# Kernel optimization log

Measured on AMD Instinct MI355X. Metric: run time of the kernel, lower is better.

## Reference

```python
import jax, jax.numpy as jnp
import numpy as np

N = 50000      # nodes
E = 400000     # edges (before self loops)
IN = 128       # in_channels
H = 4          # num_heads (layers 1-2)
C = 32         # hidden_dim per head
HID = H * C    # 128 total hidden
CLS = 40       # num_classes (out_heads = 1)
EPS = 1e-5     # BatchNorm eps
SLOPE = 0.2    # LeakyReLU negative slope (PyG GATConv default)


def setup_inputs() -> dict:
    key = jax.random.key(0)
    ks = jax.random.split(key, 24)
    rn = lambda k, shp, s: jax.random.normal(k, shp, jnp.float32) * s
    x = jax.random.normal(ks[0], (N, IN), jnp.float32)
    src = jax.random.randint(ks[1], (E,), 0, N)
    dst = jax.random.randint(ks[2], (E,), 0, N)
    src = jnp.where(src == dst, (src + 1) % N, src)  # no pre-existing self loops
    edge_index = jnp.stack([src, dst]).astype(jnp.int32)
    inp = dict(x=x, edge_index=edge_index)
    # conv1: in IN -> H heads x C
    inp['W1'] = rn(ks[3], (IN, H * C), 1.0 / np.sqrt(IN))
    inp['as1'] = rn(ks[4], (H, C), 0.1)
    inp['ad1'] = rn(ks[5], (H, C), 0.1)
    inp['b1'] = rn(ks[6], (H * C,), 0.02)
    # conv2: HID -> H x C
    inp['W2'] = rn(ks[7], (HID, H * C), 1.0 / np.sqrt(HID))
    inp['as2'] = rn(ks[8], (H, C), 0.1)
    inp['ad2'] = rn(ks[9], (H, C), 0.1)
    inp['b2'] = rn(ks[10], (H * C,), 0.02)
    # conv3: HID -> 1 head x CLS, concat=False
    inp['W3'] = rn(ks[11], (HID, CLS), 1.0 / np.sqrt(HID))
    inp['as3'] = rn(ks[12], (1, CLS), 0.1)
    inp['ad3'] = rn(ks[13], (1, CLS), 0.1)
    inp['b3'] = rn(ks[14], (CLS,), 0.02)
    # residual projection
    inp['Wres'] = rn(ks[15], (IN, HID), 1.0 / np.sqrt(IN))
    # BatchNorm (eval mode: running stats)
    inp['g1'] = 1.0 + rn(ks[16], (HID,), 0.1)
    inp['be1'] = rn(ks[17], (HID,), 0.1)
    inp['m1'] = rn(ks[18], (HID,), 0.1)
    inp['v1'] = 1.0 + jax.random.uniform(ks[19], (HID,), jnp.float32) * 0.5
    inp['g2'] = 1.0 + rn(ks[20], (HID,), 0.1)
    inp['be2'] = rn(ks[21], (HID,), 0.1)
    inp['m2'] = rn(ks[22], (HID,), 0.1)
    inp['v2'] = 1.0 + jax.random.uniform(ks[23], (HID,), jnp.float32) * 0.5
    return inp


def _gat_conv(h, src, dst, W, a_src, a_dst, bias, heads, out_ch, concat):
    """PyG-style GATConv (eval: attention dropout off), self loops already in src/dst."""
    n = h.shape[0]
    xw = (h @ W).reshape(n, heads, out_ch)                    # [N,H,C]
    e_src = jnp.sum(xw * a_src, axis=-1)                      # [N,H]
    e_dst = jnp.sum(xw * a_dst, axis=-1)                      # [N,H]
    e = jax.nn.leaky_relu(e_src[src] + e_dst[dst], SLOPE)     # [E',H]
    # segment softmax over incoming edges of each dst node
    mseg = jax.ops.segment_max(e, dst, num_segments=n)        # [N,H]
    ex = jnp.exp(e - mseg[dst])
    den = jax.ops.segment_sum(ex, dst, num_segments=n)
    alpha = ex / den[dst]                                     # [E',H]
    out = jax.ops.segment_sum(alpha[:, :, None] * xw[src], dst, num_segments=n)  # [N,H,C]
    out = out.reshape(n, heads * out_ch) if concat else out.mean(axis=1)
    return out + bias


def _bn(h, g, b, m, v):
    return (h - m) * jax.lax.rsqrt(v + EPS) * g + b


def reference(x, edge_index, W1, as1, ad1, b1, W2, as2, ad2, b2,
              W3, as3, ad3, b3, Wres, g1, be1, m1, v1, g2, be2, m2, v2):
    n = x.shape[0]
    loop = jnp.arange(n, dtype=edge_index.dtype)
    src = jnp.concatenate([edge_index[0], loop])  # add self loops (PyG default)
    dst = jnp.concatenate([edge_index[1], loop])
    x0 = x
    h = _gat_conv(x0, src, dst, W1, as1, ad1, b1, H, C, True)
    h = jax.nn.elu(_bn(h, g1, be1, m1, v1) + x0 @ Wres)
    h_res = h
    h = _gat_conv(h, src, dst, W2, as2, ad2, b2, H, C, True)
    h = jax.nn.elu(_bn(h, g2, be2, m2, v2) + h_res)
    logits = _gat_conv(h, src, dst, W3, as3, ad3, b3, 1, CLS, False)
    return logits
```

## Files before the change

### kernel.cpp

```cpp
#include <hip/hip_runtime.h>
#include <hip/hip_bf16.h>

#define THREADS 256

typedef __attribute__((ext_vector_type(8))) short bfrag;
typedef __attribute__((ext_vector_type(4))) float f32x4;

__device__ inline unsigned short f2b(float v) {
    __hip_bfloat16 b = __float2bfloat16(v);
    return *reinterpret_cast<unsigned short*>(&b);
}
__device__ inline float b2f(unsigned short u) {
    return __uint_as_float(((unsigned)u) << 16);
}
__device__ inline float rdv(const void* p, int off, bool isbf) {
    return isbf ? b2f(((const unsigned short*)p)[off]) : ((const float*)p)[off];
}

__global__ void detect_kernel(const unsigned short* __restrict__ x, int n, int* flag) {
    __shared__ int cnt;
    if (threadIdx.x == 0) cnt = 0;
    __syncthreads();
    int local = 0;
    for (int i = threadIdx.x; i < n; i += THREADS) {
        unsigned ex = (x[i] >> 7) & 0xFF;
        if (ex == 0xFF || ex >= 134 || (ex > 0 && ex <= 100)) local++;
    }
    atomicAdd(&cnt, local);
    __syncthreads();
    if (threadIdx.x == 0) *flag = (cnt * 8 > n) ? 0 : 1;
}

struct InPtrs { const void* p[23]; };

__global__ void prep_kernel(InPtrs in, const int* __restrict__ flag,
                            unsigned short* __restrict__ Wl1, unsigned short* __restrict__ Wl2,
                            unsigned short* __restrict__ WlR, unsigned short* __restrict__ Wl3,
                            float* __restrict__ bnsc1, float* __restrict__ bnsh1,
                            float* __restrict__ bnsc2, float* __restrict__ bnsh2,
                            float* __restrict__ AS1f, float* __restrict__ AD1f,
                            float* __restrict__ AS2f, float* __restrict__ AD2f,
                            float* __restrict__ AS3f, float* __restrict__ AD3f,
                            float* __restrict__ B3f, unsigned short* __restrict__ xb,
                            int N, const int* __restrict__ ei, int* __restrict__ deg,
                            int E, int CB) {
    bool isbf = (*flag != 0);
    int b = blockIdx.x;
    if (b < 27) {
        const void* Wv; unsigned short* o; int cols, tt;
        if (b < 8)       { Wv = in.p[2];  o = Wl1; cols = 128; tt = b; }
        else if (b < 16) { Wv = in.p[6];  o = Wl2; cols = 128; tt = b - 8; }
        else if (b < 24) { Wv = in.p[14]; o = WlR; cols = 128; tt = b - 16; }
        else             { Wv = in.p[10]; o = Wl3; cols = 40;  tt = b - 24; }
        int id = tt * 256 + threadIdx.x;
        int t = id >> 8, ks = (id >> 6) & 3, l = id & 63;
        int q = l >> 4, n = l & 15;
        int c = t * 16 + n;
#pragma unroll
        for (int j = 0; j < 8; ++j) {
            int k = ks * 32 + q * 8 + j;
            float v = (c < cols) ? rdv(Wv, k * cols + c, isbf) : 0.f;
            o[id * 8 + j] = f2b(v);
        }
    } else if (b == 27) {
        int c = threadIdx.x;
        if (c < 128) {
            float s = rdv(in.p[15], c, isbf) * rsqrtf(rdv(in.p[18], c, isbf) + 1e-5f);
            bnsc1[c] = s;
            bnsh1[c] = rdv(in.p[16], c, isbf) - rdv(in.p[17], c, isbf) * s +
                       rdv(in.p[5], c, isbf) * s;
            AS1f[c] = rdv(in.p[3], c, isbf);
            AD1f[c] = rdv(in.p[4], c, isbf);
            AS2f[c] = rdv(in.p[7], c, isbf);
            AD2f[c] = rdv(in.p[8], c, isbf);
        } else {
            int d = c - 128;
            float s = rdv(in.p[19], d, isbf) * rsqrtf(rdv(in.p[22], d, isbf) + 1e-5f);
            bnsc2[d] = s;
            bnsh2[d] = rdv(in.p[20], d, isbf) - rdv(in.p[21], d, isbf) * s +
                       rdv(in.p[9], d, isbf) * s;
            if (d < 40) {
                AS3f[d] = rdv(in.p[11], d, isbf);
                AD3f[d] = rdv(in.p[12], d, isbf);
                B3f[d] = rdv(in.p[13], d, isbf);
            }
        }
    } else if (b < 28 + CB) {
        int i = (b - 28) * 256 + threadIdx.x;
        if (i < E + N) {
            int d = (i < E) ? ei[E + i] : (i - E);
            atomicAdd(&deg[d], 1);
        }
    } else {
        if (isbf) return;
        const float* xf = (const float*)in.p[0];
        int total = N * 128;
        int stride = (gridDim.x - 28 - CB) * 256;
        for (int i = (b - 28 - CB) * 256 + threadIdx.x; i < total; i += stride)
            xb[i] = f2b(xf[i]);
    }
}

__global__ void bsum_kernel(const int* __restrict__ deg, int* __restrict__ bsum, int N) {
    int idx = blockIdx.x * 256 + threadIdx.x;
    int lane = threadIdx.x & 63, wv = threadIdx.x >> 6;
    int v = (idx < N) ? deg[idx] : 0;
#pragma unroll
    for (int o = 1; o < 64; o <<= 1) v += __shfl_xor(v, o, 64);
    __shared__ int ws[4];
    if (lane == 0) ws[wv] = v;
    __syncthreads();
    if (threadIdx.x == 0) bsum[blockIdx.x] = ws[0] + ws[1] + ws[2] + ws[3];
}

__global__ __launch_bounds__(1024) void bscan_kernel(const int* __restrict__ bsum,
                                                     int* __restrict__ boff, int nb) {
    __shared__ int ws[16];
    int tid = threadIdx.x, lane = tid & 63, wv = tid >> 6;
    int v = (tid < nb) ? bsum[tid] : 0;
    int sc = v;
#pragma unroll
    for (int o = 1; o < 64; o <<= 1) {
        int t = __shfl_up(sc, o, 64);
        if (lane >= o) sc += t;
    }
    if (lane == 63) ws[wv] = sc;
    __syncthreads();
    int add = 0;
#pragma unroll
    for (int k = 0; k < 16; ++k) add += (k < wv) ? ws[k] : 0;
    if (tid < nb) boff[tid] = add + sc - v;
}

__global__ void scanw_kernel(const int* __restrict__ deg, const int* __restrict__ boff,
                             int* __restrict__ row_ptr, int* __restrict__ pos, int N) {
    int idx = blockIdx.x * 256 + threadIdx.x;
    int lane = threadIdx.x & 63, wv = threadIdx.x >> 6;
    int v = (idx < N) ? deg[idx] : 0;
    int sc = v;
#pragma unroll
    for (int o = 1; o < 64; o <<= 1) {
        int t = __shfl_up(sc, o, 64);
        if (lane >= o) sc += t;
    }
    __shared__ int ws[4];
    if (lane == 63) ws[wv] = sc;
    __syncthreads();
    int add = boff[blockIdx.x];
#pragma unroll
    for (int k = 0; k < 4; ++k) add += (k < wv) ? ws[k] : 0;
    int excl = add + sc - v;
    if (idx < N) {
        pos[idx] = excl;
        row_ptr[idx + 1] = excl + v;
    }
    if (idx == 0) row_ptr[0] = 0;
}

__global__ void scatter_kernel(const int* __restrict__ ei, int* __restrict__ pos,
                               int* __restrict__ csr, int E, int N) {
    int e = blockIdx.x * THREADS + threadIdx.x;
    if (e >= E + N) return;
    int s, d;
    if (e < E) { s = ei[e]; d = ei[E + e]; }
    else { s = e - E; d = s; }
    int p = atomicAdd(&pos[d], 1);
    csr[p] = s;
}

template <int COLT, int HEADS, bool ES>
__global__ __launch_bounds__(256) void gemm_mfma(
    const unsigned short* __restrict__ A, const unsigned short* __restrict__ Wg,
    const float* __restrict__ as_f, const float* __restrict__ ad_f,
    unsigned short* __restrict__ out, int ldc, int cols,
    float* __restrict__ es, float* __restrict__ ed, int N) {
    __shared__ __align__(16) unsigned short Wls[COLT * 2048];
    int tid = threadIdx.x;
    {
        const float4* src = (const float4*)Wg;
        float4* dst = (float4*)Wls;
#pragma unroll
        for (int i = 0; i < COLT; ++i) dst[tid + i * 256] = src[tid + i * 256];
    }
    __syncthreads();
    int w = tid >> 6, lane = tid & 63;
    int n = lane & 15, q = lane >> 4;
    int row0 = blockIdx.x * 64 + w * 16;
    int ar = row0 + n; ar = ar < N ? ar : N - 1;
    f32x4 acc[COLT];
#pragma unroll
    for (int t = 0; t < COLT; ++t) acc[t] = (f32x4){0.f, 0.f, 0.f, 0.f};
    const unsigned short* arow = A + (size_t)ar * 128;
#pragma unroll
    for (int ks = 0; ks < 4; ++ks) {
        bfrag a = *reinterpret_cast<const bfrag*>(arow + ks * 32 + q * 8);
#pragma unroll
        for (int t = 0; t < COLT; ++t) {
            bfrag b = *reinterpret_cast<const bfrag*>(&Wls[((t * 4 + ks) * 64 + lane) * 8]);
            acc[t] = __builtin_amdgcn_mfma_f32_16x16x32_bf16(a, b, acc[t], 0, 0, 0);
        }
    }
    if (ES) {
        float asv[COLT], adv[COLT];
#pragma unroll
        for (int t = 0; t < COLT; ++t) {
            int c = t * 16 + n;
            asv[t] = (c < cols) ? as_f[c] : 0.f;
            adv[t] = (c < cols) ? ad_f[c] : 0.f;
        }
#pragma unroll
        for (int r = 0; r < 4; ++r) {
            float pe[HEADS], pd[HEADS];
#pragma unroll
            for (int h = 0; h < HEADS; ++h) { pe[h] = 0.f; pd[h] = 0.f; }
#pragma unroll
            for (int t = 0; t < COLT; ++t) {
                int h = (HEADS == 4) ? (t >> 1) : 0;
                pe[h] = fmaf(acc[t][r], asv[t], pe[h]);
                pd[h] = fmaf(acc[t][r], adv[t], pd[h]);
            }
#pragma unroll
            for (int h = 0; h < HEADS; ++h) {
#pragma unroll
                for (int o = 1; o < 16; o <<= 1) {
                    pe[h] += __shfl_xor(pe[h], o, 64);
                    pd[h] += __shfl_xor(pd[h], o, 64);
                }
            }
            int row = row0 + q * 4 + r;
            if (n == 0 && row < N) {
#pragma unroll
                for (int h = 0; h < HEADS; ++h) {
                    es[(size_t)row * HEADS + h] = pe[h];
                    ed[(size_t)row * HEADS + h] = pd[h];
                }
            }
        }
    }
#pragma unroll
    for (int t = 0; t < COLT; ++t) {
        int col = t * 16 + n;
        if (col < cols) {
#pragma unroll
            for (int r = 0; r < 4; ++r) {
                int row = row0 + q * 4 + r;
                if (row < N) out[(size_t)row * ldc + col] = f2b(acc[t][r]);
            }
        }
    }
}

__global__ __launch_bounds__(256) void gemm_dual(
    const unsigned short* __restrict__ Araw, const unsigned short* __restrict__ Acvt,
    const int* __restrict__ flag,
    const unsigned short* __restrict__ Wg1, const unsigned short* __restrict__ WgR,
    const float* __restrict__ as_f, const float* __restrict__ ad_f,
    unsigned short* __restrict__ xwb, unsigned short* __restrict__ resb,
    float* __restrict__ es, float* __restrict__ ed, int N) {
    __shared__ __align__(16) unsigned short Wls[16 * 2048];
    int tid = threadIdx.x;
    {
        const float4* s1 = (const float4*)Wg1;
        const float4* s2 = (const float4*)WgR;
        float4* dst = (float4*)Wls;
#pragma unroll
        for (int i = 0; i < 8; ++i) dst[tid + i * 256] = s1[tid + i * 256];
#pragma unroll
        for (int i = 0; i < 8; ++i) dst[2048 + tid + i * 256] = s2[tid + i * 256];
    }
    const unsigned short* A = (*flag) ? Araw : Acvt;
    __syncthreads();
    int w = tid >> 6, lane = tid & 63;
    int n = lane & 15, q = lane >> 4;
    int row0 = blockIdx.x * 64 + w * 16;
    int ar = row0 + n; ar = ar < N ? ar : N - 1;
    f32x4 acc[16];
#pragma unroll
    for (int t = 0; t < 16; ++t) acc[t] = (f32x4){0.f, 0.f, 0.f, 0.f};
    const unsigned short* arow = A + (size_t)ar * 128;
#pragma unroll
    for (int ks = 0; ks < 4; ++ks) {
        bfrag a = *reinterpret_cast<const bfrag*>(arow + ks * 32 + q * 8);
#pragma unroll
        for (int t = 0; t < 8; ++t) {
            bfrag b = *reinterpret_cast<const bfrag*>(&Wls[((t * 4 + ks) * 64 + lane) * 8]);
            acc[t] = __builtin_amdgcn_mfma_f32_16x16x32_bf16(a, b, acc[t], 0, 0, 0);
        }
#pragma unroll
        for (int t = 0; t < 8; ++t) {
            bfrag b = *reinterpret_cast<const bfrag*>(&Wls[16384 + ((t * 4 + ks) * 64 + lane) * 8]);
            acc[8 + t] = __builtin_amdgcn_mfma_f32_16x16x32_bf16(a, b, acc[8 + t], 0, 0, 0);
        }
    }
    float asv[8], adv[8];
#pragma unroll
    for (int t = 0; t < 8; ++t) {
        int c = t * 16 + n;
        asv[t] = as_f[c];
        adv[t] = ad_f[c];
    }
#pragma unroll
    for (int r = 0; r < 4; ++r) {
        float pe[4] = {0.f, 0.f, 0.f, 0.f}, pd[4] = {0.f, 0.f, 0.f, 0.f};
#pragma unroll
        for (int t = 0; t < 8; ++t) {
            int h = t >> 1;
            pe[h] = fmaf(acc[t][r], asv[t], pe[h]);
            pd[h] = fmaf(acc[t][r], adv[t], pd[h]);
        }
#pragma unroll
        for (int h = 0; h < 4; ++h) {
#pragma unroll
            for (int o = 1; o < 16; o <<= 1) {
                pe[h] += __shfl_xor(pe[h], o, 64);
                pd[h] += __shfl_xor(pd[h], o, 64);
            }
        }
        int row = row0 + q * 4 + r;
        if (n == 0 && row < N) {
#pragma unroll
            for (int h = 0; h < 4; ++h) {
                es[(size_t)row * 4 + h] = pe[h];
                ed[(size_t)row * 4 + h] = pd[h];
            }
        }
    }
#pragma unroll
    for (int t = 0; t < 8; ++t) {
        int col = t * 16 + n;
#pragma unroll
        for (int r = 0; r < 4; ++r) {
            int row = row0 + q * 4 + r;
            if (row < N) {
                xwb[(size_t)row * 128 + col] = f2b(acc[t][r]);
                resb[(size_t)row * 128 + col] = f2b(acc[8 + t][r]);
            }
        }
    }
}

__global__ __launch_bounds__(256) void agg128_fused(
    const unsigned short* __restrict__ xwb, const float* __restrict__ es,
    const float* __restrict__ ed, const int* __restrict__ row_ptr,
    const int* __restrict__ csr, const float* __restrict__ bnsc,
    const float* __restrict__ bnsh, const unsigned short* __restrict__ resb,
    unsigned short* __restrict__ outb, int N) {
    int w = threadIdx.x >> 6, lane = threadIdx.x & 63;
    int node = blockIdx.x * 4 + w;
    if (node >= N) return;
    int h = lane >> 4;
    int i16 = lane & 15;
    int base = lane & 48;
    int c0 = lane * 2;
    float edl = ed[node * 4 + h];
    int start = __builtin_amdgcn_readfirstlane(row_ptr[node]);
    int end = __builtin_amdgcn_readfirstlane(row_ptr[node + 1]);
    float den = 0.f, a0 = 0.f, a1 = 0.f;
    for (int jb = start; jb < end; jb += 16) {
        int cnt = end - jb; cnt = cnt < 16 ? cnt : 16;
        cnt = __builtin_amdgcn_readfirstlane(cnt);
        int idx = jb + i16;
        int sv = csr[idx < end ? idx : end - 1];
        unsigned uu[16];
#pragma unroll
        for (int u = 0; u < 16; ++u) {
            if (u < cnt) {
                int s = __shfl(sv, u, 64);
                uu[u] = *(const unsigned*)(xwb + (size_t)s * 128 + c0);
            }
        }
        float wgl = 0.f;
        if (i16 < cnt) {
            float e = es[sv * 4 + h] + edl;
            e = e > 0.f ? e : 0.2f * e;
            wgl = __expf(e);
        }
        float d = wgl;
        d += __shfl_xor(d, 1, 64);
        d += __shfl_xor(d, 2, 64);
        d += __shfl_xor(d, 4, 64);
        d += __shfl_xor(d, 8, 64);
        den += d;
#pragma unroll
        for (int u = 0; u < 16; ++u) {
            if (u < cnt) {
                float wg = __shfl(wgl, base + u, 64);
                a0 = fmaf(wg, __uint_as_float(uu[u] << 16), a0);
                a1 = fmaf(wg, __uint_as_float(uu[u] & 0xffff0000u), a1);
            }
        }
    }
    float inv = 1.f / den;
    float2 sc = *(const float2*)(bnsc + c0);
    float2 sh = *(const float2*)(bnsh + c0);
    unsigned ur = *(const unsigned*)(resb + (size_t)node * 128 + c0);
    float v0 = fmaf(a0 * inv, sc.x, sh.x) + __uint_as_float(ur << 16);
    float v1 = fmaf(a1 * inv, sc.y, sh.y) + __uint_as_float(ur & 0xffff0000u);
    v0 = v0 > 0.f ? v0 : expm1f(v0);
    v1 = v1 > 0.f ? v1 : expm1f(v1);
    unsigned pk = (unsigned)f2b(v0) | ((unsigned)f2b(v1) << 16);
    *(unsigned*)(outb + (size_t)node * 128 + c0) = pk;
}

__global__ __launch_bounds__(256) void agg40_kernel(
    const unsigned short* __restrict__ xw3b, const float* __restrict__ es3,
    const float* __restrict__ ed3, const int* __restrict__ row_ptr,
    const int* __restrict__ csr, const float* __restrict__ b3,
    void* __restrict__ out, const int* __restrict__ flag, int N) {
    int w = threadIdx.x >> 6, lane = threadIdx.x & 63;
    int node = blockIdx.x * 4 + w;
    if (node >= N) return;
    int i16 = lane & 15;
    int g = lane >= 40 ? 2 : (lane >= 20 ? 1 : 0);
    int cp = lane - g * 20;
    int c0 = cp * 2; c0 = c0 > 38 ? 38 : c0;
    float edl = ed3[node];
    int start = __builtin_amdgcn_readfirstlane(row_ptr[node]);
    int end = __builtin_amdgcn_readfirstlane(row_ptr[node + 1]);
    float den = 0.f, a0 = 0.f, a1 = 0.f;
    for (int jb = start; jb < end; jb += 16) {
        int cnt = end - jb; cnt = cnt < 16 ? cnt : 16;
        cnt = __builtin_amdgcn_readfirstlane(cnt);
        int idx = jb + i16;
        int sv = csr[idx < end ? idx : end - 1];
        unsigned uu[6];
#pragma unroll
        for (int t = 0; t < 6; ++t) {
            int slot = 3 * t + g;
            if (slot < cnt) {
                int s = __shfl(sv, slot, 64);
                uu[t] = *(const unsigned*)(xw3b + (size_t)s * 40 + c0);
            }
        }
        float wgl = 0.f;
        if (i16 < cnt) {
            float e = es3[sv] + edl;
            e = e > 0.f ? e : 0.2f * e;
            wgl = __expf(e);
        }
        float d = wgl;
        d += __shfl_xor(d, 1, 64);
        d += __shfl_xor(d, 2, 64);
        d += __shfl_xor(d, 4, 64);
        d += __shfl_xor(d, 8, 64);
        den += d;
#pragma unroll
        for (int t = 0; t < 6; ++t) {
            int slot = 3 * t + g;
            if (slot < cnt) {
                float wg = __shfl(wgl, slot, 64);
                a0 = fmaf(wg, __uint_as_float(uu[t] << 16), a0);
                a1 = fmaf(wg, __uint_as_float(uu[t] & 0xffff0000u), a1);
            }
        }
    }
    float t0 = __shfl(a0, (lane + 20) & 63, 64);
    float t1 = __shfl(a0, (lane + 40) & 63, 64);
    float u0 = __shfl(a1, (lane + 20) & 63, 64);
    float u1 = __shfl(a1, (lane + 40) & 63, 64);
    a0 += t0 + t1;
    a1 += u0 + u1;
    if (lane < 20) {
        float inv = 1.f / den;
        float v0 = a0 * inv + b3[c0];
        float v1 = a1 * inv + b3[c0 + 1];
        size_t eoff = (size_t)node * 40 + c0;
        if (*flag) {
            unsigned pk = (unsigned)f2b(v0) | ((unsigned)f2b(v1) << 16);
            *(unsigned*)((unsigned short*)out + eoff) = pk;
        } else {
            *(float2*)((float*)out + eoff) = make_float2(v0, v1);
        }
    }
}

extern "C" void kernel_launch(void* const* d_in, const int* in_sizes, int n_in,
                              void* d_out, int out_size, void* d_ws, size_t ws_size,
                              hipStream_t stream) {
    (void)n_in; (void)out_size; (void)ws_size;
    const int N = in_sizes[0] / 128;
    const int E = in_sizes[1] / 2;
    const int EPN = E + N;
    const int NB = (N + 255) / 256;
    const int CB = (EPN + 255) / 256;
    char* base = (char*)d_ws;
    size_t off = 0;
    auto alloc = [&](size_t bytes) -> char* {
        char* p = base + off;
        off = (off + bytes + 255) & ~(size_t)255;
        return p;
    };
    int* flag = (int*)alloc(4);
    int* deg = (int*)alloc((size_t)N * 4);
    int* row_ptr = (int*)alloc((size_t)(N + 1) * 4);
    int* pos = (int*)alloc((size_t)N * 4);
    int* bsum = (int*)alloc((size_t)NB * 4);
    int* boff = (int*)alloc((size_t)NB * 4);
    int* csr = (int*)alloc((size_t)EPN * 4);
    float* bnsc1 = (float*)alloc(512); float* bnsh1 = (float*)alloc(512);
    float* bnsc2 = (float*)alloc(512); float* bnsh2 = (float*)alloc(512);
    float* AS1f = (float*)alloc(512); float* AD1f = (float*)alloc(512);
    float* AS2f = (float*)alloc(512); float* AD2f = (float*)alloc(512);
    float* AS3f = (float*)alloc(256); float* AD3f = (float*)alloc(256);
    float* B3f = (float*)alloc(256);
    unsigned short* Wl1 = (unsigned short*)alloc(32768);
    unsigned short* Wl2 = (unsigned short*)alloc(32768);
    unsigned short* WlR = (unsigned short*)alloc(32768);
    unsigned short* Wl3 = (unsigned short*)alloc(12288);
    unsigned short* xb = (unsigned short*)alloc((size_t)N * 128 * 2);
    unsigned short* xwb = (unsigned short*)alloc((size_t)N * 128 * 2);
    unsigned short* h1b = (unsigned short*)alloc((size_t)N * 128 * 2);
    unsigned short* resb = (unsigned short*)alloc((size_t)N * 128 * 2);
    float* es = (float*)alloc((size_t)N * 4 * 4);
    float* ed = (float*)alloc((size_t)N * 4 * 4);

    const int* ei = (const int*)d_in[1];

    hipMemsetAsync(deg, 0, (size_t)N * 4, stream);
    detect_kernel<<<1, THREADS, 0, stream>>>((const unsigned short*)d_in[0], 4096, flag);

    InPtrs ip;
    for (int t = 0; t < 23; t++) ip.p[t] = d_in[t];
    prep_kernel<<<28 + CB + 1024, THREADS, 0, stream>>>(ip, flag, Wl1, Wl2, WlR, Wl3,
                                                        bnsc1, bnsh1, bnsc2, bnsh2,
                                                        AS1f, AD1f, AS2f, AD2f,
                                                        AS3f, AD3f, B3f, xb, N, ei, deg, E, CB);

    bsum_kernel<<<NB, 256, 0, stream>>>(deg, bsum, N);
    bscan_kernel<<<1, 1024, 0, stream>>>(bsum, boff, NB);
    scanw_kernel<<<NB, 256, 0, stream>>>(deg, boff, row_ptr, pos, N);
    scatter_kernel<<<(EPN + THREADS - 1) / THREADS, THREADS, 0, stream>>>(ei, pos, csr, E, N);

    int gemmGrid = (N + 63) / 64;
    int aggGrid = (N + 3) / 4;

    gemm_dual<<<gemmGrid, 256, 0, stream>>>((const unsigned short*)d_in[0], xb, flag,
                                            Wl1, WlR, AS1f, AD1f, xwb, resb, es, ed, N);
    agg128_fused<<<aggGrid, 256, 0, stream>>>(xwb, es, ed, row_ptr, csr,
                                              bnsc1, bnsh1, resb, h1b, N);
    gemm_mfma<8, 4, true><<<gemmGrid, 256, 0, stream>>>(
        h1b, Wl2, AS2f, AD2f, xwb, 128, 128, es, ed, N);
    unsigned short* h2b = resb;
    agg128_fused<<<aggGrid, 256, 0, stream>>>(xwb, es, ed, row_ptr, csr,
                                              bnsc2, bnsh2, h1b, h2b, N);
    gemm_mfma<3, 1, true><<<gemmGrid, 256, 0, stream>>>(
        h2b, Wl3, AS3f, AD3f, xwb, 40, 40, es, ed, N);
    agg40_kernel<<<aggGrid, 256, 0, stream>>>(xwb, es, ed, row_ptr, csr, B3f,
                                              d_out, flag, N);
}
```

Measured before the change: 332.5 us.

## Split 128-wide aggregation into four per-head passes over head-blocked feature layout

Stores the projected features, residuals and hidden activations in a head-blocked layout ([4][N][32] bf16) and stores attention logits head-major. The 128-wide aggregation becomes four launches, one per head, with two nodes per wavefront. Each pass gathers only a 3.2 MB slice, which is meant to stay cache-resident and improve gather locality. The cost is four times as many launches, repeated CSR and row_ptr reads per pass, and unmasked gathers that waste work on partial neighbour chunks. The final aggregation also drops its readfirstlane and branch guards in favour of clamped, masked loads.

After: 326.7 us. No clear change (-1.8%).

```diff
diff --git a/kernel.cpp b/kernel.cpp
--- a/kernel.cpp
+++ b/kernel.cpp
@@ -168,12 +168,13 @@
     csr[p] = s;
 }
 
-template <int COLT, int HEADS, bool ES>
+template <int COLT, int HEADS, bool ES, bool CBLK>
 __global__ __launch_bounds__(256) void gemm_mfma(
     const unsigned short* __restrict__ A, const unsigned short* __restrict__ Wg,
     const float* __restrict__ as_f, const float* __restrict__ ad_f,
     unsigned short* __restrict__ out, int ldc, int cols,
-    float* __restrict__ es, float* __restrict__ ed, int N) {
+    float* __restrict__ es, float* __restrict__ ed, int N,
+    long aRow, long aKs) {
     __shared__ __align__(16) unsigned short Wls[COLT * 2048];
     int tid = threadIdx.x;
     {
@@ -190,10 +191,10 @@
     f32x4 acc[COLT];
 #pragma unroll
     for (int t = 0; t < COLT; ++t) acc[t] = (f32x4){0.f, 0.f, 0.f, 0.f};
-    const unsigned short* arow = A + (size_t)ar * 128;
+    const unsigned short* abase = A + (size_t)ar * aRow;
 #pragma unroll
     for (int ks = 0; ks < 4; ++ks) {
-        bfrag a = *reinterpret_cast<const bfrag*>(arow + ks * 32 + q * 8);
+        bfrag a = *reinterpret_cast<const bfrag*>(abase + (size_t)ks * aKs + q * 8);
 #pragma unroll
         for (int t = 0; t < COLT; ++t) {
             bfrag b = *reinterpret_cast<const bfrag*>(&Wls[((t * 4 + ks) * 64 + lane) * 8]);
@@ -231,8 +232,8 @@
             if (n == 0 && row < N) {
 #pragma unroll
                 for (int h = 0; h < HEADS; ++h) {
-                    es[(size_t)row * HEADS + h] = pe[h];
-                    ed[(size_t)row * HEADS + h] = pd[h];
+                    es[(size_t)h * N + row] = pe[h];
+                    ed[(size_t)h * N + row] = pd[h];
                 }
             }
         }
@@ -244,7 +245,13 @@
 #pragma unroll
             for (int r = 0; r < 4; ++r) {
                 int row = row0 + q * 4 + r;
-                if (row < N) out[(size_t)row * ldc + col] = f2b(acc[t][r]);
+                if (row < N) {
+                    if (CBLK)
+                        out[(size_t)(col >> 5) * N * 32 + (size_t)row * 32 + (col & 31)] =
+                            f2b(acc[t][r]);
+                    else
+                        out[(size_t)row * ldc + col] = f2b(acc[t][r]);
+                }
             }
         }
     }
@@ -320,8 +327,8 @@
         if (n == 0 && row < N) {
 #pragma unroll
             for (int h = 0; h < 4; ++h) {
-                es[(size_t)row * 4 + h] = pe[h];
-                ed[(size_t)row * 4 + h] = pd[h];
+                es[(size_t)h * N + row] = pe[h];
+                ed[(size_t)h * N + row] = pd[h];
             }
         }
     }
@@ -332,46 +339,44 @@
         for (int r = 0; r < 4; ++r) {
             int row = row0 + q * 4 + r;
             if (row < N) {
-                xwb[(size_t)row * 128 + col] = f2b(acc[t][r]);
-                resb[(size_t)row * 128 + col] = f2b(acc[8 + t][r]);
-            }
-        }
-    }
-}
-
-__global__ __launch_bounds__(256) void agg128_fused(
+                size_t o = (size_t)(col >> 5) * N * 32 + (size_t)row * 32 + (col & 31);
+                xwb[o] = f2b(acc[t][r]);
+                resb[o] = f2b(acc[8 + t][r]);
+            }
+        }
+    }
+}
+
+__global__ __launch_bounds__(256) void agg128_pass(
     const unsigned short* __restrict__ xwb, const float* __restrict__ es,
     const float* __restrict__ ed, const int* __restrict__ row_ptr,
     const int* __restrict__ csr, const float* __restrict__ bnsc,
     const float* __restrict__ bnsh, const unsigned short* __restrict__ resb,
-    unsigned short* __restrict__ outb, int N) {
-    int w = threadIdx.x >> 6, lane = threadIdx.x & 63;
-    int node = blockIdx.x * 4 + w;
+    unsigned short* __restrict__ outb, int N, int pass) {
+    int tid = threadIdx.x;
+    int w = tid >> 6, lane = tid & 63;
+    int half = lane >> 5, grp2 = (lane >> 4) & 1, l16 = lane & 15;
+    int node = (blockIdx.x * 4 + w) * 2 + half;
     if (node >= N) return;
-    int h = lane >> 4;
-    int i16 = lane & 15;
-    int base = lane & 48;
-    int c0 = lane * 2;
-    float edl = ed[node * 4 + h];
-    int start = __builtin_amdgcn_readfirstlane(row_ptr[node]);
-    int end = __builtin_amdgcn_readfirstlane(row_ptr[node + 1]);
+    const unsigned short* xh = xwb + (size_t)pass * N * 32;
+    const float* esh = es + (size_t)pass * N;
+    float edl = ed[(size_t)pass * N + node];
+    int start = row_ptr[node], end = row_ptr[node + 1];
+    int c0 = l16 * 2;
     float den = 0.f, a0 = 0.f, a1 = 0.f;
     for (int jb = start; jb < end; jb += 16) {
         int cnt = end - jb; cnt = cnt < 16 ? cnt : 16;
-        cnt = __builtin_amdgcn_readfirstlane(cnt);
-        int idx = jb + i16;
+        int idx = jb + l16;
         int sv = csr[idx < end ? idx : end - 1];
-        unsigned uu[16];
-#pragma unroll
-        for (int u = 0; u < 16; ++u) {
-            if (u < cnt) {
-                int s = __shfl(sv, u, 64);
-                uu[u] = *(const unsigned*)(xwb + (size_t)s * 128 + c0);
-            }
+        unsigned uu[8];
+#pragma unroll
+        for (int u = 0; u < 8; ++u) {
+            int s = __shfl(sv, half * 32 + grp2 * 8 + u, 64);
+            uu[u] = *(const unsigned*)(xh + (size_t)s * 32 + c0);
         }
         float wgl = 0.f;
-        if (i16 < cnt) {
-            float e = es[sv * 4 + h] + edl;
+        if (l16 < cnt) {
+            float e = esh[sv] + edl;
             e = e > 0.f ? e : 0.2f * e;
             wgl = __expf(e);
         }
@@ -382,24 +387,28 @@
         d += __shfl_xor(d, 8, 64);
         den += d;
 #pragma unroll
-        for (int u = 0; u < 16; ++u) {
-            if (u < cnt) {
-                float wg = __shfl(wgl, base + u, 64);
-                a0 = fmaf(wg, __uint_as_float(uu[u] << 16), a0);
-                a1 = fmaf(wg, __uint_as_float(uu[u] & 0xffff0000u), a1);
-            }
-        }
-    }
-    float inv = 1.f / den;
-    float2 sc = *(const float2*)(bnsc + c0);
-    float2 sh = *(const float2*)(bnsh + c0);
-    unsigned ur = *(const unsigned*)(resb + (size_t)node * 128 + c0);
-    float v0 = fmaf(a0 * inv, sc.x, sh.x) + __uint_as_float(ur << 16);
-    float v1 = fmaf(a1 * inv, sc.y, sh.y) + __uint_as_float(ur & 0xffff0000u);
-    v0 = v0 > 0.f ? v0 : expm1f(v0);
-    v1 = v1 > 0.f ? v1 : expm1f(v1);
-    unsigned pk = (unsigned)f2b(v0) | ((unsigned)f2b(v1) << 16);
-    *(unsigned*)(outb + (size_t)node * 128 + c0) = pk;
+        for (int u = 0; u < 8; ++u) {
+            float wg = __shfl(wgl, half * 32 + grp2 * 8 + u, 64);
+            a0 = fmaf(wg, __uint_as_float(uu[u] << 16), a0);
+            a1 = fmaf(wg, __uint_as_float(uu[u] & 0xffff0000u), a1);
+        }
+    }
+    a0 += __shfl_xor(a0, 16, 64);
+    a1 += __shfl_xor(a1, 16, 64);
+    if (grp2 == 0) {
+        int cg = pass * 32 + c0;
+        float inv = 1.f / den;
+        float2 sc = *(const float2*)(bnsc + cg);
+        float2 sh = *(const float2*)(bnsh + cg);
+        size_t ro = ((size_t)pass * N + node) * 32 + c0;
+        unsigned ur = *(const unsigned*)(resb + ro);
+        float v0 = fmaf(a0 * inv, sc.x, sh.x) + __uint_as_float(ur << 16);
+        float v1 = fmaf(a1 * inv, sc.y, sh.y) + __uint_as_float(ur & 0xffff0000u);
+        v0 = v0 > 0.f ? v0 : expm1f(v0);
+        v1 = v1 > 0.f ? v1 : expm1f(v1);
+        unsigned pk = (unsigned)f2b(v0) | ((unsigned)f2b(v1) << 16);
+        *(unsigned*)(outb + ro) = pk;
+    }
 }
 
 __global__ __launch_bounds__(256) void agg40_kernel(
@@ -415,22 +424,17 @@
     int cp = lane - g * 20;
     int c0 = cp * 2; c0 = c0 > 38 ? 38 : c0;
     float edl = ed3[node];
-    int start = __builtin_amdgcn_readfirstlane(row_ptr[node]);
-    int end = __builtin_amdgcn_readfirstlane(row_ptr[node + 1]);
+    int start = row_ptr[node], end = row_ptr[node + 1];
     float den = 0.f, a0 = 0.f, a1 = 0.f;
     for (int jb = start; jb < end; jb += 16) {
         int cnt = end - jb; cnt = cnt < 16 ? cnt : 16;
-        cnt = __builtin_amdgcn_readfirstlane(cnt);
-        int idx = jb + i16;
-        int sv = csr[idx < end ? idx : end - 1];
+        int sv = csr[jb + (i16 < cnt ? i16 : 0)];
         unsigned uu[6];
 #pragma unroll
         for (int t = 0; t < 6; ++t) {
-            int slot = 3 * t + g;
-            if (slot < cnt) {
-                int s = __shfl(sv, slot, 64);
-                uu[t] = *(const unsigned*)(xw3b + (size_t)s * 40 + c0);
-            }
+            int slot = 3 * t + g; slot = slot < 15 ? slot : 15;
+            int s = __shfl(sv, slot, 64);
+            uu[t] = *(const unsigned*)(xw3b + (size_t)s * 40 + c0);
         }
         float wgl = 0.f;
         if (i16 < cnt) {
@@ -447,11 +451,11 @@
 #pragma unroll
         for (int t = 0; t < 6; ++t) {
             int slot = 3 * t + g;
-            if (slot < cnt) {
-                float wg = __shfl(wgl, slot, 64);
-                a0 = fmaf(wg, __uint_as_float(uu[t] << 16), a0);
-                a1 = fmaf(wg, __uint_as_float(uu[t] & 0xffff0000u), a1);
-            }
+            int sl = slot < 15 ? slot : 15;
+            float wg = __shfl(wgl, sl, 64);
+            if (slot >= cnt) wg = 0.f;
+            a0 = fmaf(wg, __uint_as_float(uu[t] << 16), a0);
+            a1 = fmaf(wg, __uint_as_float(uu[t] & 0xffff0000u), a1);
         }
     }
     float t0 = __shfl(a0, (lane + 20) & 63, 64);
@@ -532,19 +536,22 @@
     scatter_kernel<<<(EPN + THREADS - 1) / THREADS, THREADS, 0, stream>>>(ei, pos, csr, E, N);
 
     int gemmGrid = (N + 63) / 64;
+    int passGrid = (N + 7) / 8;
     int aggGrid = (N + 3) / 4;
 
     gemm_dual<<<gemmGrid, 256, 0, stream>>>((const unsigned short*)d_in[0], xb, flag,
                                             Wl1, WlR, AS1f, AD1f, xwb, resb, es, ed, N);
-    agg128_fused<<<aggGrid, 256, 0, stream>>>(xwb, es, ed, row_ptr, csr,
-                                              bnsc1, bnsh1, resb, h1b, N);
-    gemm_mfma<8, 4, true><<<gemmGrid, 256, 0, stream>>>(
-        h1b, Wl2, AS2f, AD2f, xwb, 128, 128, es, ed, N);
+    for (int p = 0; p < 4; ++p)
+        agg128_pass<<<passGrid, 256, 0, stream>>>(xwb, es, ed, row_ptr, csr,
+                                                  bnsc1, bnsh1, resb, h1b, N, p);
+    gemm_mfma<8, 4, true, true><<<gemmGrid, 256, 0, stream>>>(
+        h1b, Wl2, AS2f, AD2f, xwb, 128, 128, es, ed, N, 32L, (long)N * 32);
     unsigned short* h2b = resb;
-    agg128_fused<<<aggGrid, 256, 0, stream>>>(xwb, es, ed, row_ptr, csr,
-                                              bnsc2, bnsh2, h1b, h2b, N);
-    gemm_mfma<3, 1, true><<<gemmGrid, 256, 0, stream>>>(
-        h2b, Wl3, AS3f, AD3f, xwb, 40, 40, es, ed, N);
+    for (int p = 0; p < 4; ++p)
+        agg128_pass<<<passGrid, 256, 0, stream>>>(xwb, es, ed, row_ptr, csr,
+                                                  bnsc2, bnsh2, h1b, h2b, N, p);
+    gemm_mfma<3, 1, true, false><<<gemmGrid, 256, 0, stream>>>(
+        h2b, Wl3, AS3f, AD3f, xwb, 40, 40, es, ed, N, 32L, (long)N * 32);
     agg40_kernel<<<aggGrid, 256, 0, stream>>>(xwb, es, ed, row_ptr, csr, B3f,
                                               d_out, flag, N);
 }
```
